# Kernel optimization log

Measured on AMD Instinct MI355X. Metric: run time of the kernel, lower is better.

Reference implementation:

```python
import jax, jax.numpy as jnp
import numpy as np

HIDDEN = 2048
N_EXPERTS = 8
TOP_K = 2
MOE_INTER = 1408
NORM_TOPK = False  # config.norm_topk_prob


def setup_inputs() -> dict:
    key = jax.random.key(0)
    k0, k1, k2, k3, k4 = jax.random.split(key, 5)
    hidden_states = jax.random.normal(k0, (2, 2048, HIDDEN), dtype=jnp.float32)
    # router gate: nn.Linear(hidden, num_experts, bias=False) -> store as [H, E]
    gate_w = jax.random.normal(k1, (HIDDEN, N_EXPERTS), dtype=jnp.float32) * 0.02
    # per-expert MLP weights, stacked over experts (Linear is x @ W.T, stored pre-transposed)
    w_gate = jax.random.normal(k2, (N_EXPERTS, HIDDEN, MOE_INTER), dtype=jnp.float32) * 0.02
    w_up = jax.random.normal(k3, (N_EXPERTS, HIDDEN, MOE_INTER), dtype=jnp.float32) * 0.02
    w_down = jax.random.normal(k4, (N_EXPERTS, MOE_INTER, HIDDEN), dtype=jnp.float32) * 0.02
    return {"hidden_states": hidden_states, "gate_w": gate_w,
            "w_gate": w_gate, "w_up": w_up, "w_down": w_down}


def reference(hidden_states, gate_w, w_gate, w_up, w_down):
    B, S, H = hidden_states.shape
    x = hidden_states.reshape(-1, H)                      # [T, H]
    T = x.shape[0]
    router_logits = x @ gate_w                            # [T, E]
    probs = jax.nn.softmax(router_logits.astype(jnp.float32), axis=-1)
    routing_weights, selected = jax.lax.top_k(probs, TOP_K)  # [T, K], [T, K]
    if NORM_TOPK:
        routing_weights = routing_weights / routing_weights.sum(-1, keepdims=True)
    routing_weights = routing_weights.astype(x.dtype)
    # dense combine weights [T, E]: scatter top-k weights to expert slots
    combine = jnp.zeros((T, N_EXPERTS), dtype=x.dtype)
    combine = combine.at[jnp.arange(T)[:, None], selected].add(routing_weights)
    # run all experts densely (reference form of gather-MLP-scatter)
    g = jnp.einsum('th,ehf->tef', x, w_gate)              # [T, E, F]
    u = jnp.einsum('th,ehf->tef', x, w_up)
    h = jax.nn.silu(g) * u
    y = jnp.einsum('tef,efh->teh', h, w_down)             # [T, E, H]
    out = jnp.einsum('te,teh->th', combine, y)            # [T, H]
    return out
```

## Files before the change

### kernel.cpp

```cpp
#include <hip/hip_runtime.h>
#include <hip/hip_bf16.h>

#define HID  2048
#define NEXP 8
#define FINT 1408
#define TM   256
#define BK   32
#define GU_NPAN 88
#define DN_NPAN 64

typedef __bf16 bf16_t;
typedef __bf16 bf16x8 __attribute__((ext_vector_type(8)));
typedef float  f32x4  __attribute__((ext_vector_type(4)));

#define AS1 __attribute__((address_space(1)))
#define AS3 __attribute__((address_space(3)))

__device__ __forceinline__ void gll16(const void* g, void* l) {
    __builtin_amdgcn_global_load_lds((const AS1 void*)g, (AS3 void*)l, 16, 0, 0);
}

#define VMCNT4() asm volatile("s_waitcnt vmcnt(4)" ::: "memory")
#define VMCNT0() asm volatile("s_waitcnt vmcnt(0)" ::: "memory")
#define LGKM0()  asm volatile("s_waitcnt lgkmcnt(0)" ::: "memory")
#define SB0() __builtin_amdgcn_sched_barrier(0)

__global__ __launch_bounds__(64) void router_kernel(
    const float* __restrict__ x, const float* __restrict__ gw,
    int* __restrict__ cnt, int* __restrict__ topk_id, float* __restrict__ topk_w,
    bf16_t* __restrict__ xb, int T)
{
    int t = blockIdx.x;
    if (t >= T) return;
    int lane = threadIdx.x;
    float acc[NEXP];
#pragma unroll
    for (int e = 0; e < NEXP; ++e) acc[e] = 0.f;
    const float* xr = x + (size_t)t * HID;
    bf16_t* xo = xb + (size_t)t * HID;
    for (int i = lane; i < HID; i += 64) {
        float xv = xr[i];
        xo[i] = (bf16_t)xv;
        const float4* g4 = (const float4*)(gw + (size_t)i * NEXP);
        float4 a = g4[0], b = g4[1];
        acc[0] += xv * a.x; acc[1] += xv * a.y; acc[2] += xv * a.z; acc[3] += xv * a.w;
        acc[4] += xv * b.x; acc[5] += xv * b.y; acc[6] += xv * b.z; acc[7] += xv * b.w;
    }
#pragma unroll
    for (int d = 1; d < 64; d <<= 1) {
#pragma unroll
        for (int e = 0; e < NEXP; ++e) acc[e] += __shfl_xor(acc[e], d, 64);
    }
    float mx = acc[0];
#pragma unroll
    for (int e = 1; e < NEXP; ++e) mx = fmaxf(mx, acc[e]);
    float p[NEXP]; float s = 0.f;
#pragma unroll
    for (int e = 0; e < NEXP; ++e) { p[e] = expf(acc[e] - mx); s += p[e]; }
    float inv = 1.f / s;
    int i1 = 0;
#pragma unroll
    for (int e = 1; e < NEXP; ++e) if (acc[e] > acc[i1]) i1 = e;
    int i2 = (i1 == 0) ? 1 : 0;
#pragma unroll
    for (int e = 0; e < NEXP; ++e) if (e != i1 && acc[e] > acc[i2]) i2 = e;
    if (lane == 0) {
        topk_id[t * 2 + 0] = i1; topk_id[t * 2 + 1] = i2;
        topk_w[t * 2 + 0] = p[i1] * inv; topk_w[t * 2 + 1] = p[i2] * inv;
        atomicAdd(&cnt[i1], 1); atomicAdd(&cnt[i2], 1);
    }
}

__global__ void offsets_kernel(const int* __restrict__ cnt, int* __restrict__ offs,
                               int* __restrict__ gbase, int* __restrict__ gcount,
                               int* __restrict__ dbase, int* __restrict__ dcount,
                               int* __restrict__ gu, int* __restrict__ dn)
{
    __shared__ int gc[8], dc[8];
    int tid = threadIdx.x;
    if (tid == 0) {
        int s = 0;
        for (int e = 0; e < NEXP; ++e) { offs[e] = s; s += cnt[e]; }
        offs[NEXP] = s;
    }
    if (tid < 8) {
        int c = 0;
        for (int p = tid; p < GU_NPAN; p += 8) { int e = p / 11; c += (cnt[e] + TM - 1) / TM; }
        gc[tid] = c;
    } else if (tid < 16) {
        int x = tid - 8, c = 0;
        for (int p = x; p < DN_NPAN; p += 8) { int e = p >> 3; c += (cnt[e] + TM - 1) / TM; }
        dc[x] = c;
    }
    __syncthreads();
    if (tid < 8) {
        int base = 0;
        for (int i = 0; i < tid; ++i) base += gc[i];
        gbase[tid] = base; gcount[tid] = gc[tid];
        int k = base;
        for (int p = tid; p < GU_NPAN; p += 8) {
            int e = p / 11, fp = p - e * 11;
            int nt = (cnt[e] + TM - 1) / TM;
            for (int t = 0; t < nt; ++t) gu[k++] = (e << 10) | (fp << 6) | t;
        }
    } else if (tid < 16) {
        int x = tid - 8;
        int base = 0;
        for (int i = 0; i < x; ++i) base += dc[i];
        dbase[x] = base; dcount[x] = dc[x];
        int k = base;
        for (int p = x; p < DN_NPAN; p += 8) {
            int e = p >> 3, hp = p & 7;
            int nt = (cnt[e] + TM - 1) / TM;
            for (int t = 0; t < nt; ++t) dn[k++] = (e << 10) | (hp << 6) | t;
        }
    }
}

__global__ void scatter_kernel(
    const int* __restrict__ topk_id, const int* __restrict__ offs, int* __restrict__ fill,
    int* __restrict__ tok, int* __restrict__ slot_of, int T)
{
    int t = blockIdx.x * blockDim.x + threadIdx.x;
    if (t >= T) return;
#pragma unroll
    for (int k = 0; k < 2; ++k) {
        int e = topk_id[t * 2 + k];
        int pos = atomicAdd(&fill[e], 1);
        int slot = offs[e] + pos;
        tok[slot] = t;
        slot_of[t * 2 + k] = slot;
    }
}

__global__ __launch_bounds__(256) void cvt3_kernel(
    const float* __restrict__ wg, const float* __restrict__ wu, const float* __restrict__ wd,
    bf16_t* __restrict__ wgb, bf16_t* __restrict__ wub, bf16_t* __restrict__ wdb)
{
    const int per = NEXP * (HID / 64) * (FINT / 64);
    int b = blockIdx.x;
    const float* in; bf16_t* outb; int R, C;
    if (b < per)            { in = wg; outb = wgb; R = HID;  C = FINT; }
    else if (b < 2 * per)   { b -= per; in = wu; outb = wub; R = HID;  C = FINT; }
    else                    { b -= 2 * per; in = wd; outb = wdb; R = FINT; C = HID; }

    int tilesC = C >> 6;
    int perE = (R >> 6) * tilesC;
    int e = b / perE;
    int rem = b - e * perE;
    int tr = rem / tilesC, tc = rem - tr * tilesC;
    const float* src = in + (size_t)e * R * C + (size_t)(tr * 64) * C + tc * 64;
    bf16_t* dst = outb + (size_t)e * R * C + (size_t)(tc * 64) * R + tr * 64;

    __shared__ float tile[64][65];
    int tid = threadIdx.x;
    int rr = tid >> 4;
    int cc = (tid & 15) * 4;
#pragma unroll
    for (int i = 0; i < 4; ++i) {
        float4 v = *(const float4*)(src + (size_t)(rr + i * 16) * C + cc);
        tile[rr + i * 16][cc + 0] = v.x; tile[rr + i * 16][cc + 1] = v.y;
        tile[rr + i * 16][cc + 2] = v.z; tile[rr + i * 16][cc + 3] = v.w;
    }
    __syncthreads();
    int oc = tid >> 2;
    int og = (tid & 3) * 16;
    bf16_t* dp = dst + (size_t)oc * R + og;
    bf16x8 o0, o1;
#pragma unroll
    for (int j = 0; j < 8; ++j) { o0[j] = (bf16_t)tile[og + j][oc]; o1[j] = (bf16_t)tile[og + 8 + j][oc]; }
    *(bf16x8*)dp = o0;
    *(bf16x8*)(dp + 8) = o1;
}

__global__ __launch_bounds__(512, 2) void gateup3_kernel(
    const bf16_t* __restrict__ xb, const bf16_t* __restrict__ wgb, const bf16_t* __restrict__ wub,
    const int* __restrict__ offs, const int* __restrict__ tok,
    const int* __restrict__ gbase, const int* __restrict__ gcount, const int* __restrict__ gu,
    bf16_t* __restrict__ h_buf)
{
    __shared__ bf16_t smem[49152];
    const int tid = threadIdx.x;
    const int lane = tid & 63, w = tid >> 6;
    const int wm = w >> 1, wn = w & 1;
    const int lr = lane & 15, lg = lane >> 4;
    const int rl = lane >> 2;
    const int sw8 = ((lane & 3) ^ ((lane >> 3) & 3)) * 8;
    const int ksw = (lg ^ ((lr >> 1) & 3)) * 8;

    const int xcd = blockIdx.x & 7, slot = blockIdx.x >> 3;
    const int icnt = gcount[xcd], ib = gbase[xcd];

    for (int ii = slot; ii < icnt; ii += 32) {
        const int it = gu[ib + ii];
        const int e = it >> 10, fp = (it >> 6) & 15, tr = it & 63;
        const int seg0 = offs[e];
        const int rbase = tr * TM;
        const int nvalid = min(offs[e + 1] - seg0 - rbase, TM);
        const int row0 = seg0 + rbase;
        const int f0 = fp * 128;

        const bf16_t* aP[2];
#pragma unroll
        for (int i = 0; i < 2; ++i) {
            int r = (w * 2 + i) * 16 + rl;
            int tk = tok[row0 + min(r, nvalid - 1)];
            aP[i] = xb + (size_t)tk * HID + sw8;
        }
        const bf16_t* bP[2];
#pragma unroll
        for (int i = 0; i < 2; ++i) {
            int br = (w * 2 + i) * 16 + rl;
            const bf16_t* W = (br < 128) ? wgb : wub;
            bP[i] = W + ((size_t)e * FINT + f0 + (br & 127)) * HID + sw8;
        }

        f32x4 acc[4][8];
#pragma unroll
        for (int mi = 0; mi < 4; ++mi)
#pragma unroll
            for (int ni = 0; ni < 8; ++ni) acc[mi][ni] = (f32x4){0.f, 0.f, 0.f, 0.f};

        auto STAGE_A = [&](int b, int kt) {
            int k0 = kt * BK;
            bf16_t* A = smem + b * 8192;
            gll16(aP[0] + k0, A + (w * 2 + 0) * 512);
            gll16(aP[1] + k0, A + (w * 2 + 1) * 512);
        };
        auto STAGE_B = [&](int b, int kt) {
            int k0 = kt * BK;
            bf16_t* B = smem + 24576 + b * 8192;
            gll16(bP[0] + k0, B + (w * 2 + 0) * 512);
            gll16(bP[1] + k0, B + (w * 2 + 1) * 512);
        };

        const int NK = HID / BK;
        STAGE_A(0, 0); STAGE_B(0, 0); STAGE_A(1, 1); STAGE_B(1, 1);
        int c0 = 0, c1 = 1, c2 = 2;
        for (int kt = 0; kt < NK; ++kt) {
            SB0();
            if (kt + 1 < NK) { VMCNT4(); } else { VMCNT0(); }
            __builtin_amdgcn_s_barrier();
            SB0();
            const bf16_t* A = smem + c0 * 8192;
            const bf16_t* B = smem + 24576 + c0 * 8192;
            if (kt + 2 < NK) STAGE_A(c2, kt + 2);
            bf16x8 afr[4], bfr[4];
#pragma unroll
            for (int mi = 0; mi < 4; ++mi)
                afr[mi] = *(const bf16x8*)&A[(wm * 64 + mi * 16 + lr) * BK + ksw];
#pragma unroll
            for (int ni = 0; ni < 4; ++ni)
                bfr[ni] = *(const bf16x8*)&B[(wn * 128 + ni * 16 + lr) * BK + ksw];
            LGKM0(); SB0();
            __builtin_amdgcn_s_setprio(1);
#pragma unroll
            for (int mi = 0; mi < 4; ++mi)
#pragma unroll
                for (int ni = 0; ni < 4; ++ni)
                    acc[mi][ni] = __builtin_amdgcn_mfma_f32_16x16x32_bf16(afr[mi], bfr[ni], acc[mi][ni], 0, 0, 0);
            __builtin_amdgcn_s_setprio(0);
            SB0();
            if (kt + 2 < NK) STAGE_B(c2, kt + 2);
#pragma unroll
            for (int ni = 0; ni < 4; ++ni)
                bfr[ni] = *(const bf16x8*)&B[(wn * 128 + (ni + 4) * 16 + lr) * BK + ksw];
            LGKM0(); SB0();
            __builtin_amdgcn_s_setprio(1);
#pragma unroll
            for (int mi = 0; mi < 4; ++mi)
#pragma unroll
                for (int ni = 0; ni < 4; ++ni)
                    acc[mi][ni + 4] = __builtin_amdgcn_mfma_f32_16x16x32_bf16(afr[mi], bfr[ni], acc[mi][ni + 4], 0, 0, 0);
            __builtin_amdgcn_s_setprio(0);
            SB0();
            int t = c0; c0 = c1; c1 = c2; c2 = t;
        }
        __syncthreads();

        if (wn == 1) {
#pragma unroll
            for (int mi = 0; mi < 4; ++mi)
#pragma unroll
                for (int ni = 0; ni < 8; ++ni)
#pragma unroll
                    for (int rr = 0; rr < 4; ++rr) {
                        int row = wm * 64 + mi * 16 + lg * 4 + rr;
                        int col = ni * 16 + lr;
                        smem[row * 128 + col] = (bf16_t)acc[mi][ni][rr];
                    }
        }
        __syncthreads();
        if (wn == 0) {
#pragma unroll
            for (int mi = 0; mi < 4; ++mi)
#pragma unroll
                for (int ni = 0; ni < 8; ++ni)
#pragma unroll
                    for (int rr = 0; rr < 4; ++rr) {
                        int row = wm * 64 + mi * 16 + lg * 4 + rr;
                        int col = ni * 16 + lr;
                        float g = acc[mi][ni][rr];
                        float u = (float)smem[row * 128 + col];
                        float h = (g / (1.f + __expf(-g))) * u;
                        if (row < nvalid)
                            h_buf[(size_t)(row0 + row) * FINT + f0 + col] = (bf16_t)h;
                    }
        }
        __syncthreads();
    }
}

__global__ __launch_bounds__(512, 2) void down3_kernel(
    const bf16_t* __restrict__ h_buf, const bf16_t* __restrict__ wdb,
    const int* __restrict__ offs,
    const int* __restrict__ dbase, const int* __restrict__ dcount, const int* __restrict__ dn,
    bf16_t* __restrict__ y_buf)
{
    __shared__ bf16_t smem[49152];
    const int tid = threadIdx.x;
    const int lane = tid & 63, w = tid >> 6;
    const int wm = w >> 1, wn = w & 1;
    const int lr = lane & 15, lg = lane >> 4;
    const int rl = lane >> 2;
    const int sw8 = ((lane & 3) ^ ((lane >> 3) & 3)) * 8;
    const int ksw = (lg ^ ((lr >> 1) & 3)) * 8;

    const int xcd = blockIdx.x & 7, slot = blockIdx.x >> 3;
    const int icnt = dcount[xcd], ib = dbase[xcd];

    for (int ii = slot; ii < icnt; ii += 32) {
        const int it = dn[ib + ii];
        const int e = it >> 10, hp = (it >> 6) & 15, tr = it & 63;
        const int seg0 = offs[e];
        const int rbase = tr * TM;
        const int nvalid = min(offs[e + 1] - seg0 - rbase, TM);
        const int row0 = seg0 + rbase;
        const int h0 = hp * 256;

        const bf16_t* aP[2];
#pragma unroll
        for (int i = 0; i < 2; ++i) {
            int r = (w * 2 + i) * 16 + rl;
            aP[i] = h_buf + (size_t)(row0 + r) * FINT + sw8;
        }
        const bf16_t* bP[2];
#pragma unroll
        for (int i = 0; i < 2; ++i) {
            int br = (w * 2 + i) * 16 + rl;
            bP[i] = wdb + ((size_t)e * HID + h0 + br) * FINT + sw8;
        }

        f32x4 acc[4][8];
#pragma unroll
        for (int mi = 0; mi < 4; ++mi)
#pragma unroll
            for (int ni = 0; ni < 8; ++ni) acc[mi][ni] = (f32x4){0.f, 0.f, 0.f, 0.f};

        auto STAGE_A = [&](int b, int kt) {
            int k0 = kt * BK;
            bf16_t* A = smem + b * 8192;
            gll16(aP[0] + k0, A + (w * 2 + 0) * 512);
            gll16(aP[1] + k0, A + (w * 2 + 1) * 512);
        };
        auto STAGE_B = [&](int b, int kt) {
            int k0 = kt * BK;
            bf16_t* B = smem + 24576 + b * 8192;
            gll16(bP[0] + k0, B + (w * 2 + 0) * 512);
            gll16(bP[1] + k0, B + (w * 2 + 1) * 512);
        };

        const int NK = FINT / BK;
        STAGE_A(0, 0); STAGE_B(0, 0); STAGE_A(1, 1); STAGE_B(1, 1);
        int c0 = 0, c1 = 1, c2 = 2;
        for (int kt = 0; kt < NK; ++kt) {
            SB0();
            if (kt + 1 < NK) { VMCNT4(); } else { VMCNT0(); }
            __builtin_amdgcn_s_barrier();
            SB0();
            const bf16_t* A = smem + c0 * 8192;
            const bf16_t* B = smem + 24576 + c0 * 8192;
            if (kt + 2 < NK) STAGE_A(c2, kt + 2);
            bf16x8 afr[4], bfr[4];
#pragma unroll
            for (int mi = 0; mi < 4; ++mi)
                afr[mi] = *(const bf16x8*)&A[(wm * 64 + mi * 16 + lr) * BK + ksw];
#pragma unroll
            for (int ni = 0; ni < 4; ++ni)
                bfr[ni] = *(const bf16x8*)&B[(wn * 128 + ni * 16 + lr) * BK + ksw];
            LGKM0(); SB0();
            __builtin_amdgcn_s_setprio(1);
#pragma unroll
            for (int mi = 0; mi < 4; ++mi)
#pragma unroll
                for (int ni = 0; ni < 4; ++ni)
                    acc[mi][ni] = __builtin_amdgcn_mfma_f32_16x16x32_bf16(afr[mi], bfr[ni], acc[mi][ni], 0, 0, 0);
            __builtin_amdgcn_s_setprio(0);
            SB0();
            if (kt + 2 < NK) STAGE_B(c2, kt + 2);
#pragma unroll
            for (int ni = 0; ni < 4; ++ni)
                bfr[ni] = *(const bf16x8*)&B[(wn * 128 + (ni + 4) * 16 + lr) * BK + ksw];
            LGKM0(); SB0();
            __builtin_amdgcn_s_setprio(1);
#pragma unroll
            for (int mi = 0; mi < 4; ++mi)
#pragma unroll
                for (int ni = 0; ni < 4; ++ni)
                    acc[mi][ni + 4] = __builtin_amdgcn_mfma_f32_16x16x32_bf16(afr[mi], bfr[ni], acc[mi][ni + 4], 0, 0, 0);
            __builtin_amdgcn_s_setprio(0);
            SB0();
            int t = c0; c0 = c1; c1 = c2; c2 = t;
        }

#pragma unroll
        for (int mi = 0; mi < 4; ++mi)
#pragma unroll
            for (int ni = 0; ni < 8; ++ni)
#pragma unroll
                for (int rr = 0; rr < 4; ++rr) {
                    int row = wm * 64 + mi * 16 + lg * 4 + rr;
                    int col = wn * 128 + ni * 16 + lr;
                    if (row < nvalid)
                        y_buf[(size_t)(row0 + row) * HID + h0 + col] = (bf16_t)acc[mi][ni][rr];
                }
        __syncthreads();
    }
}

__global__ __launch_bounds__(256) void combine_kernel(
    const bf16_t* __restrict__ y, const int* __restrict__ slot_of,
    const float* __restrict__ topk_w, float* __restrict__ out, int T)
{
    int t = blockIdx.x;
    int tid = threadIdx.x;
    int s0 = slot_of[t * 2], s1 = slot_of[t * 2 + 1];
    float w0 = topk_w[t * 2], w1 = topk_w[t * 2 + 1];
    const bf16x8* y0 = (const bf16x8*)(y + (size_t)s0 * HID);
    const bf16x8* y1 = (const bf16x8*)(y + (size_t)s1 * HID);
    bf16x8 v0 = y0[tid], v1 = y1[tid];
    float* op = out + (size_t)t * HID + tid * 8;
#pragma unroll
    for (int j = 0; j < 8; ++j)
        op[j] = w0 * (float)v0[j] + w1 * (float)v1[j];
}

extern "C" void kernel_launch(void* const* d_in, const int* in_sizes, int n_in,
                              void* d_out, int out_size, void* d_ws, size_t ws_size,
                              hipStream_t stream)
{
    const float* x  = (const float*)d_in[0];
    const float* gw = (const float*)d_in[1];
    const float* wg = (const float*)d_in[2];
    const float* wu = (const float*)d_in[3];
    const float* wd = (const float*)d_in[4];
    float* out = (float*)d_out;
    int T = in_sizes[0] / HID;
    int S2 = 2 * T;

    char* base = (char*)d_ws;
    int* cnt     = (int*)base;
    int* fill    = cnt + 8;
    int* offs    = cnt + 16;
    int* gbase   = cnt + 32;
    int* gcount  = cnt + 40;
    int* dbase   = cnt + 48;
    int* dcount  = cnt + 56;
    int* gu      = cnt + 64;
    int* dnl     = cnt + 576;
    int* topk_id = cnt + 960;
    float* topk_w = (float*)(topk_id + S2);
    int* tok     = (int*)(topk_w + S2);
    int* slot_of = tok + S2 + 256;
    size_t small_end = (size_t)((char*)(slot_of + S2) - base);
    size_t cur = (small_end + 255) & ~(size_t)255;
    auto take = [&](size_t bytes) -> size_t {
        size_t o = cur; cur += bytes; cur = (cur + 255) & ~(size_t)255; return o;
    };
    size_t wbytes = (size_t)NEXP * HID * FINT * 2;
    size_t o_xb  = take((size_t)T * HID * 2);
    size_t o_wgb = take(wbytes);
    size_t o_wub = take(wbytes);
    size_t o_wdb = take(wbytes);
    size_t o_h   = take((size_t)(S2 + 256) * FINT * 2);
    size_t o_y   = take((size_t)(S2 + 256) * HID * 2);
    (void)ws_size;

    bf16_t* xb    = (bf16_t*)(base + o_xb);
    bf16_t* wgb   = (bf16_t*)(base + o_wgb);
    bf16_t* wub   = (bf16_t*)(base + o_wub);
    bf16_t* wdb   = (bf16_t*)(base + o_wdb);
    bf16_t* h_buf = (bf16_t*)(base + o_h);
    bf16_t* y_buf = (bf16_t*)(base + o_y);

    hipMemsetAsync(base, 0, 64, stream);

    router_kernel<<<T, 64, 0, stream>>>(x, gw, cnt, topk_id, topk_w, xb, T);
    offsets_kernel<<<1, 64, 0, stream>>>(cnt, offs, gbase, gcount, dbase, dcount, gu, dnl);
    scatter_kernel<<<(T + 255) / 256, 256, 0, stream>>>(topk_id, offs, fill, tok, slot_of, T);

    int gridW = 3 * NEXP * (HID / 64) * (FINT / 64);
    cvt3_kernel<<<gridW, 256, 0, stream>>>(wg, wu, wd, wgb, wub, wdb);

    gateup3_kernel<<<256, 512, 0, stream>>>(xb, wgb, wub, offs, tok, gbase, gcount, gu, h_buf);
    down3_kernel<<<256, 512, 0, stream>>>(h_buf, wdb, offs, dbase, dcount, dnl, y_buf);
    combine_kernel<<<T, 256, 0, stream>>>(y_buf, slot_of, topk_w, out, T);
}
```

Before: 469.4 us.

## Restructure grouped GEMMs to BK=64 quadrant-pipelined double buffering with 2x4 warp grid

Both the gate/up and down grouped GEMM kernels move from a BK=32 triple-buffered loop to BK=64 double buffering with 128 KB of LDS. Each k-step is split into four quadrant sub-tiles whose loads are staged in between the MFMA phases. Warps are rearranged as a 2x4 grid with a 128x64 tile per warp, and the LDS swizzle becomes 8-way XOR. The aim is fewer barriers per unit of MFMA work and less wasted global-load issue, at the cost of dropping to one block per CU. The router kernel also switches to float4 loads of x.

```diff
diff --git a/kernel.cpp b/kernel.cpp
--- a/kernel.cpp
+++ b/kernel.cpp
@@ -5,7 +5,6 @@
 #define NEXP 8
 #define FINT 1408
 #define TM   256
-#define BK   32
 #define GU_NPAN 88
 #define DN_NPAN 64
 
@@ -20,8 +19,9 @@
     __builtin_amdgcn_global_load_lds((const AS1 void*)g, (AS3 void*)l, 16, 0, 0);
 }
 
-#define VMCNT4() asm volatile("s_waitcnt vmcnt(4)" ::: "memory")
-#define VMCNT0() asm volatile("s_waitcnt vmcnt(0)" ::: "memory")
+#define VM4() asm volatile("s_waitcnt vmcnt(4)" ::: "memory")
+#define VM2() asm volatile("s_waitcnt vmcnt(2)" ::: "memory")
+#define VM0() asm volatile("s_waitcnt vmcnt(0)" ::: "memory")
 #define LGKM0()  asm volatile("s_waitcnt lgkmcnt(0)" ::: "memory")
 #define SB0() __builtin_amdgcn_sched_barrier(0)
 
@@ -38,13 +38,18 @@
     for (int e = 0; e < NEXP; ++e) acc[e] = 0.f;
     const float* xr = x + (size_t)t * HID;
     bf16_t* xo = xb + (size_t)t * HID;
-    for (int i = lane; i < HID; i += 64) {
-        float xv = xr[i];
-        xo[i] = (bf16_t)xv;
-        const float4* g4 = (const float4*)(gw + (size_t)i * NEXP);
-        float4 a = g4[0], b = g4[1];
-        acc[0] += xv * a.x; acc[1] += xv * a.y; acc[2] += xv * a.z; acc[3] += xv * a.w;
-        acc[4] += xv * b.x; acc[5] += xv * b.y; acc[6] += xv * b.z; acc[7] += xv * b.w;
+    for (int i0 = lane * 4; i0 < HID; i0 += 256) {
+        float4 xv = *(const float4*)(xr + i0);
+        bf16_t b4[4] = {(bf16_t)xv.x, (bf16_t)xv.y, (bf16_t)xv.z, (bf16_t)xv.w};
+        *(uint2*)(xo + i0) = *(uint2*)b4;
+        float xs[4] = {xv.x, xv.y, xv.z, xv.w};
+#pragma unroll
+        for (int u = 0; u < 4; ++u) {
+            const float4* g4 = (const float4*)(gw + (size_t)(i0 + u) * NEXP);
+            float4 a = g4[0], b = g4[1];
+            acc[0] += xs[u] * a.x; acc[1] += xs[u] * a.y; acc[2] += xs[u] * a.z; acc[3] += xs[u] * a.w;
+            acc[4] += xs[u] * b.x; acc[5] += xs[u] * b.y; acc[6] += xs[u] * b.z; acc[7] += xs[u] * b.w;
+        }
     }
 #pragma unroll
     for (int d = 1; d < 64; d <<= 1) {
@@ -173,20 +178,24 @@
     *(bf16x8*)(dp + 8) = o1;
 }
 
-__global__ __launch_bounds__(512, 2) void gateup3_kernel(
+
+__global__ __launch_bounds__(512, 1) void gateup4_kernel(
     const bf16_t* __restrict__ xb, const bf16_t* __restrict__ wgb, const bf16_t* __restrict__ wub,
     const int* __restrict__ offs, const int* __restrict__ tok,
     const int* __restrict__ gbase, const int* __restrict__ gcount, const int* __restrict__ gu,
     bf16_t* __restrict__ h_buf)
 {
-    __shared__ bf16_t smem[49152];
+    __shared__ bf16_t smem[65536];
     const int tid = threadIdx.x;
     const int lane = tid & 63, w = tid >> 6;
-    const int wm = w >> 1, wn = w & 1;
+    const int wr = w >> 2, wc = w & 3;
     const int lr = lane & 15, lg = lane >> 4;
-    const int rl = lane >> 2;
-    const int sw8 = ((lane & 3) ^ ((lane >> 3) & 3)) * 8;
-    const int ksw = (lg ^ ((lr >> 1) & 3)) * 8;
+    const int sw7 = lr & 7;
+    const int ksrc = ((lane & 7) ^ ((lane >> 3) & 7)) * 8;
+    int iS[2];
+#pragma unroll
+    for (int j = 0; j < 2; ++j) iS[j] = w * 16 + j * 8 + (lane >> 3);
+    const int dA[2] = { (w * 128 + 0) * 8, (w * 128 + 64) * 8 };
 
     const int xcd = blockIdx.x & 7, slot = blockIdx.x >> 3;
     const int icnt = gcount[xcd], ib = gbase[xcd];
@@ -200,107 +209,109 @@
         const int row0 = seg0 + rbase;
         const int f0 = fp * 128;
 
-        const bf16_t* aP[2];
-#pragma unroll
-        for (int i = 0; i < 2; ++i) {
-            int r = (w * 2 + i) * 16 + rl;
-            int tk = tok[row0 + min(r, nvalid - 1)];
-            aP[i] = xb + (size_t)tk * HID + sw8;
-        }
-        const bf16_t* bP[2];
-#pragma unroll
-        for (int i = 0; i < 2; ++i) {
-            int br = (w * 2 + i) * 16 + rl;
-            const bf16_t* W = (br < 128) ? wgb : wub;
-            bP[i] = W + ((size_t)e * FINT + f0 + (br & 127)) * HID + sw8;
-        }
-
-        f32x4 acc[4][8];
-#pragma unroll
-        for (int mi = 0; mi < 4; ++mi)
-#pragma unroll
-            for (int ni = 0; ni < 8; ++ni) acc[mi][ni] = (f32x4){0.f, 0.f, 0.f, 0.f};
-
-        auto STAGE_A = [&](int b, int kt) {
-            int k0 = kt * BK;
-            bf16_t* A = smem + b * 8192;
-            gll16(aP[0] + k0, A + (w * 2 + 0) * 512);
-            gll16(aP[1] + k0, A + (w * 2 + 1) * 512);
+        const bf16_t* aSrc[2][2];
+        const bf16_t* bSrc[2];
+#pragma unroll
+        for (int j = 0; j < 2; ++j) {
+            int rA0 = ((iS[j] >> 6) << 7) + (iS[j] & 63);
+#pragma unroll
+            for (int mh = 0; mh < 2; ++mh) {
+                int rA = rA0 + mh * 64;
+                int tk = tok[row0 + min(rA, nvalid - 1)];
+                aSrc[j][mh] = xb + (size_t)tk * HID + ksrc;
+            }
+            int rB = ((iS[j] >> 5) << 6) + (iS[j] & 31);
+            const bf16_t* W = (rB < 128) ? wgb : wub;
+            bSrc[j] = W + ((size_t)e * FINT + f0 + (rB & 127)) * HID + ksrc;
+        }
+
+        f32x4 acc[8][4];
+#pragma unroll
+        for (int mf = 0; mf < 8; ++mf)
+#pragma unroll
+            for (int nf = 0; nf < 4; ++nf) acc[mf][nf] = (f32x4){0.f, 0.f, 0.f, 0.f};
+
+        auto SG_A = [&](int bb, int kt, int mh) {
+#pragma unroll
+            for (int j = 0; j < 2; ++j)
+                gll16(aSrc[j][mh] + kt * 64, &smem[bb * 16384 + mh * 8192 + dA[j]]);
         };
-        auto STAGE_B = [&](int b, int kt) {
-            int k0 = kt * BK;
-            bf16_t* B = smem + 24576 + b * 8192;
-            gll16(bP[0] + k0, B + (w * 2 + 0) * 512);
-            gll16(bP[1] + k0, B + (w * 2 + 1) * 512);
+        auto SG_B = [&](int bb, int kt, int nh) {
+#pragma unroll
+            for (int j = 0; j < 2; ++j)
+                gll16(bSrc[j] + (size_t)nh * 32 * HID + kt * 64, &smem[32768 + bb * 16384 + nh * 8192 + dA[j]]);
         };
 
-        const int NK = HID / BK;
-        STAGE_A(0, 0); STAGE_B(0, 0); STAGE_A(1, 1); STAGE_B(1, 1);
-        int c0 = 0, c1 = 1, c2 = 2;
+#define GU_READ_MFMA(BB, MH, NH)                                                              \
+        {                                                                                     \
+            bf16x8 afr[4][2], bfr[2][2];                                                      \
+            _Pragma("unroll")                                                                 \
+            for (int m = 0; m < 4; ++m)                                                       \
+                _Pragma("unroll")                                                             \
+                for (int ks = 0; ks < 2; ++ks)                                                \
+                    afr[m][ks] = *(const bf16x8*)&smem[(BB) * 16384 + (MH) * 8192 +           \
+                        (wr * 64 + m * 16 + lr) * 64 + (((ks * 4 + lg) ^ sw7)) * 8];          \
+            _Pragma("unroll")                                                                 \
+            for (int n = 0; n < 2; ++n)                                                       \
+                _Pragma("unroll")                                                             \
+                for (int ks = 0; ks < 2; ++ks)                                                \
+                    bfr[n][ks] = *(const bf16x8*)&smem[32768 + (BB) * 16384 + (NH) * 8192 +   \
+                        (wc * 32 + n * 16 + lr) * 64 + (((ks * 4 + lg) ^ sw7)) * 8];          \
+            LGKM0(); SB0();                                                                   \
+            __builtin_amdgcn_s_setprio(1);                                                    \
+            _Pragma("unroll")                                                                 \
+            for (int m = 0; m < 4; ++m)                                                       \
+                _Pragma("unroll")                                                             \
+                for (int n = 0; n < 2; ++n)                                                   \
+                    _Pragma("unroll")                                                         \
+                    for (int ks = 0; ks < 2; ++ks)                                            \
+                        acc[(MH) * 4 + m][(NH) * 2 + n] = __builtin_amdgcn_mfma_f32_16x16x32_bf16( \
+                            afr[m][ks], bfr[n][ks], acc[(MH) * 4 + m][(NH) * 2 + n], 0, 0, 0); \
+            __builtin_amdgcn_s_setprio(0);                                                    \
+        }
+
+        const int NK = HID / 64;
+        SG_B(0, 0, 0); SG_A(0, 0, 0); SG_A(0, 0, 1); SG_B(0, 0, 1);
         for (int kt = 0; kt < NK; ++kt) {
-            SB0();
-            if (kt + 1 < NK) { VMCNT4(); } else { VMCNT0(); }
-            __builtin_amdgcn_s_barrier();
-            SB0();
-            const bf16_t* A = smem + c0 * 8192;
-            const bf16_t* B = smem + 24576 + c0 * 8192;
-            if (kt + 2 < NK) STAGE_A(c2, kt + 2);
-            bf16x8 afr[4], bfr[4];
-#pragma unroll
-            for (int mi = 0; mi < 4; ++mi)
-                afr[mi] = *(const bf16x8*)&A[(wm * 64 + mi * 16 + lr) * BK + ksw];
-#pragma unroll
-            for (int ni = 0; ni < 4; ++ni)
-                bfr[ni] = *(const bf16x8*)&B[(wn * 128 + ni * 16 + lr) * BK + ksw];
-            LGKM0(); SB0();
-            __builtin_amdgcn_s_setprio(1);
-#pragma unroll
-            for (int mi = 0; mi < 4; ++mi)
-#pragma unroll
-                for (int ni = 0; ni < 4; ++ni)
-                    acc[mi][ni] = __builtin_amdgcn_mfma_f32_16x16x32_bf16(afr[mi], bfr[ni], acc[mi][ni], 0, 0, 0);
-            __builtin_amdgcn_s_setprio(0);
-            SB0();
-            if (kt + 2 < NK) STAGE_B(c2, kt + 2);
-#pragma unroll
-            for (int ni = 0; ni < 4; ++ni)
-                bfr[ni] = *(const bf16x8*)&B[(wn * 128 + (ni + 4) * 16 + lr) * BK + ksw];
-            LGKM0(); SB0();
-            __builtin_amdgcn_s_setprio(1);
-#pragma unroll
-            for (int mi = 0; mi < 4; ++mi)
-#pragma unroll
-                for (int ni = 0; ni < 4; ++ni)
-                    acc[mi][ni + 4] = __builtin_amdgcn_mfma_f32_16x16x32_bf16(afr[mi], bfr[ni], acc[mi][ni + 4], 0, 0, 0);
-            __builtin_amdgcn_s_setprio(0);
-            SB0();
-            int t = c0; c0 = c1; c1 = c2; c2 = t;
+            const int bb = kt & 1, nb = bb ^ 1;
+            const bool nl = (kt + 1 < NK);
+            SB0(); LGKM0(); VM4(); __builtin_amdgcn_s_barrier(); SB0();
+            if (nl) SG_B(nb, kt + 1, 0);
+            GU_READ_MFMA(bb, 0, 0);
+            SB0(); LGKM0(); if (nl) { VM4(); } else { VM2(); } __builtin_amdgcn_s_barrier(); SB0();
+            if (nl) SG_A(nb, kt + 1, 0);
+            GU_READ_MFMA(bb, 1, 0);
+            SB0(); LGKM0(); if (nl) { VM4(); } else { VM0(); } __builtin_amdgcn_s_barrier(); SB0();
+            if (nl) SG_A(nb, kt + 1, 1);
+            GU_READ_MFMA(bb, 0, 1);
+            if (nl) SG_B(nb, kt + 1, 1);
+            GU_READ_MFMA(bb, 1, 1);
         }
         __syncthreads();
 
-        if (wn == 1) {
-#pragma unroll
-            for (int mi = 0; mi < 4; ++mi)
-#pragma unroll
-                for (int ni = 0; ni < 8; ++ni)
+        if (wc >= 2) {
+#pragma unroll
+            for (int mf = 0; mf < 8; ++mf)
+#pragma unroll
+                for (int nf = 0; nf < 4; ++nf)
 #pragma unroll
                     for (int rr = 0; rr < 4; ++rr) {
-                        int row = wm * 64 + mi * 16 + lg * 4 + rr;
-                        int col = ni * 16 + lr;
-                        smem[row * 128 + col] = (bf16_t)acc[mi][ni][rr];
+                        int row = wr * 128 + mf * 16 + lg * 4 + rr;
+                        int col = (wc - 2) * 64 + nf * 16 + lr;
+                        smem[row * 128 + col] = (bf16_t)acc[mf][nf][rr];
                     }
         }
         __syncthreads();
-        if (wn == 0) {
-#pragma unroll
-            for (int mi = 0; mi < 4; ++mi)
-#pragma unroll
-                for (int ni = 0; ni < 8; ++ni)
+        if (wc < 2) {
+#pragma unroll
+            for (int mf = 0; mf < 8; ++mf)
+#pragma unroll
+                for (int nf = 0; nf < 4; ++nf)
 #pragma unroll
                     for (int rr = 0; rr < 4; ++rr) {
-                        int row = wm * 64 + mi * 16 + lg * 4 + rr;
-                        int col = ni * 16 + lr;
-                        float g = acc[mi][ni][rr];
+                        int row = wr * 128 + mf * 16 + lg * 4 + rr;
+                        int col = wc * 64 + nf * 16 + lr;
+                        float g = acc[mf][nf][rr];
                         float u = (float)smem[row * 128 + col];
                         float h = (g / (1.f + __expf(-g))) * u;
                         if (row < nvalid)
@@ -309,22 +320,26 @@
         }
         __syncthreads();
     }
-}
-
-__global__ __launch_bounds__(512, 2) void down3_kernel(
+#undef GU_READ_MFMA
+}
+
+__global__ __launch_bounds__(512, 1) void down4_kernel(
     const bf16_t* __restrict__ h_buf, const bf16_t* __restrict__ wdb,
     const int* __restrict__ offs,
     const int* __restrict__ dbase, const int* __restrict__ dcount, const int* __restrict__ dn,
     bf16_t* __restrict__ y_buf)
 {
-    __shared__ bf16_t smem[49152];
+    __shared__ bf16_t smem[65536];
     const int tid = threadIdx.x;
     const int lane = tid & 63, w = tid >> 6;
-    const int wm = w >> 1, wn = w & 1;
+    const int wr = w >> 2, wc = w & 3;
     const int lr = lane & 15, lg = lane >> 4;
-    const int rl = lane >> 2;
-    const int sw8 = ((lane & 3) ^ ((lane >> 3) & 3)) * 8;
-    const int ksw = (lg ^ ((lr >> 1) & 3)) * 8;
+    const int sw7 = lr & 7;
+    const int ksrc = ((lane & 7) ^ ((lane >> 3) & 7)) * 8;
+    int iS[2];
+#pragma unroll
+    for (int j = 0; j < 2; ++j) iS[j] = w * 16 + j * 8 + (lane >> 3);
+    const int dA[2] = { (w * 128 + 0) * 8, (w * 128 + 64) * 8 };
 
     const int xcd = blockIdx.x & 7, slot = blockIdx.x >> 3;
     const int icnt = dcount[xcd], ib = dbase[xcd];
@@ -338,94 +353,95 @@
         const int row0 = seg0 + rbase;
         const int h0 = hp * 256;
 
-        const bf16_t* aP[2];
-#pragma unroll
-        for (int i = 0; i < 2; ++i) {
-            int r = (w * 2 + i) * 16 + rl;
-            aP[i] = h_buf + (size_t)(row0 + r) * FINT + sw8;
-        }
-        const bf16_t* bP[2];
-#pragma unroll
-        for (int i = 0; i < 2; ++i) {
-            int br = (w * 2 + i) * 16 + rl;
-            bP[i] = wdb + ((size_t)e * HID + h0 + br) * FINT + sw8;
-        }
-
-        f32x4 acc[4][8];
-#pragma unroll
-        for (int mi = 0; mi < 4; ++mi)
-#pragma unroll
-            for (int ni = 0; ni < 8; ++ni) acc[mi][ni] = (f32x4){0.f, 0.f, 0.f, 0.f};
-
-        auto STAGE_A = [&](int b, int kt) {
-            int k0 = kt * BK;
-            bf16_t* A = smem + b * 8192;
-            gll16(aP[0] + k0, A + (w * 2 + 0) * 512);
-            gll16(aP[1] + k0, A + (w * 2 + 1) * 512);
+        const bf16_t* aSrc[2][2];
+        const bf16_t* bSrc[2];
+#pragma unroll
+        for (int j = 0; j < 2; ++j) {
+            int rA0 = ((iS[j] >> 6) << 7) + (iS[j] & 63);
+#pragma unroll
+            for (int mh = 0; mh < 2; ++mh)
+                aSrc[j][mh] = h_buf + (size_t)(row0 + rA0 + mh * 64) * FINT + ksrc;
+            int rB = ((iS[j] >> 5) << 6) + (iS[j] & 31);
+            bSrc[j] = wdb + ((size_t)e * HID + h0 + rB) * FINT + ksrc;
+        }
+
+        f32x4 acc[8][4];
+#pragma unroll
+        for (int mf = 0; mf < 8; ++mf)
+#pragma unroll
+            for (int nf = 0; nf < 4; ++nf) acc[mf][nf] = (f32x4){0.f, 0.f, 0.f, 0.f};
+
+        auto SG_A = [&](int bb, int kt, int mh) {
+#pragma unroll
+            for (int j = 0; j < 2; ++j)
+                gll16(aSrc[j][mh] + kt * 64, &smem[bb * 16384 + mh * 8192 + dA[j]]);
         };
-        auto STAGE_B = [&](int b, int kt) {
-            int k0 = kt * BK;
-            bf16_t* B = smem + 24576 + b * 8192;
-            gll16(bP[0] + k0, B + (w * 2 + 0) * 512);
-            gll16(bP[1] + k0, B + (w * 2 + 1) * 512);
+        auto SG_B = [&](int bb, int kt, int nh) {
+#pragma unroll
+            for (int j = 0; j < 2; ++j)
+                gll16(bSrc[j] + (size_t)nh * 32 * FINT + kt * 64, &smem[32768 + bb * 16384 + nh * 8192 + dA[j]]);
         };
 
-        const int NK = FINT / BK;
-        STAGE_A(0, 0); STAGE_B(0, 0); STAGE_A(1, 1); STAGE_B(1, 1);
-        int c0 = 0, c1 = 1, c2 = 2;
+#define DN_READ_MFMA(BB, MH, NH)                                                              \
+        {                                                                                     \
+            bf16x8 afr[4][2], bfr[2][2];                                                      \
+            _Pragma("unroll")                                                                 \
+            for (int m = 0; m < 4; ++m)                                                       \
+                _Pragma("unroll")                                                             \
+                for (int ks = 0; ks < 2; ++ks)                                                \
+                    afr[m][ks] = *(const bf16x8*)&smem[(BB) * 16384 + (MH) * 8192 +           \
+                        (wr * 64 + m * 16 + lr) * 64 + (((ks * 4 + lg) ^ sw7)) * 8];          \
+            _Pragma("unroll")                                                                 \
+            for (int n = 0; n < 2; ++n)                                                       \
+                _Pragma("unroll")                                                             \
+                for (int ks = 0; ks < 2; ++ks)                                                \
+                    bfr[n][ks] = *(const bf16x8*)&smem[32768 + (BB) * 16384 + (NH) * 8192 +   \
+                        (wc * 32 + n * 16 + lr) * 64 + (((ks * 4 + lg) ^ sw7)) * 8];          \
+            LGKM0(); SB0();                                                                   \
+            __builtin_amdgcn_s_setprio(1);                                                    \
+            _Pragma("unroll")                                                                 \
+            for (int m = 0; m < 4; ++m)                                                       \
+                _Pragma("unroll")                                                             \
+                for (int n = 0; n < 2; ++n)                                                   \
+                    _Pragma("unroll")                                                         \
+                    for (int ks = 0; ks < 2; ++ks)                                            \
+                        acc[(MH) * 4 + m][(NH) * 2 + n] = __builtin_amdgcn_mfma_f32_16x16x32_bf16( \
+                            afr[m][ks], bfr[n][ks], acc[(MH) * 4 + m][(NH) * 2 + n], 0, 0, 0); \
+            __builtin_amdgcn_s_setprio(0);                                                    \
+        }
+
+        const int NK = FINT / 64;
+        SG_B(0, 0, 0); SG_A(0, 0, 0); SG_A(0, 0, 1); SG_B(0, 0, 1);
         for (int kt = 0; kt < NK; ++kt) {
-            SB0();
-            if (kt + 1 < NK) { VMCNT4(); } else { VMCNT0(); }
-            __builtin_amdgcn_s_barrier();
-            SB0();
-            const bf16_t* A = smem + c0 * 8192;
-            const bf16_t* B = smem + 24576 + c0 * 8192;
-            if (kt + 2 < NK) STAGE_A(c2, kt + 2);
-            bf16x8 afr[4], bfr[4];
-#pragma unroll
-            for (int mi = 0; mi < 4; ++mi)
-                afr[mi] = *(const bf16x8*)&A[(wm * 64 + mi * 16 + lr) * BK + ksw];
-#pragma unroll
-            for (int ni = 0; ni < 4; ++ni)
-                bfr[ni] = *(const bf16x8*)&B[(wn * 128 + ni * 16 + lr) * BK + ksw];
-            LGKM0(); SB0();
-            __builtin_amdgcn_s_setprio(1);
-#pragma unroll
-            for (int mi = 0; mi < 4; ++mi)
-#pragma unroll
-                for (int ni = 0; ni < 4; ++ni)
-                    acc[mi][ni] = __builtin_amdgcn_mfma_f32_16x16x32_bf16(afr[mi], bfr[ni], acc[mi][ni], 0, 0, 0);
-            __builtin_amdgcn_s_setprio(0);
-            SB0();
-            if (kt + 2 < NK) STAGE_B(c2, kt + 2);
-#pragma unroll
-            for (int ni = 0; ni < 4; ++ni)
-                bfr[ni] = *(const bf16x8*)&B[(wn * 128 + (ni + 4) * 16 + lr) * BK + ksw];
-            LGKM0(); SB0();
-            __builtin_amdgcn_s_setprio(1);
-#pragma unroll
-            for (int mi = 0; mi < 4; ++mi)
-#pragma unroll
-                for (int ni = 0; ni < 4; ++ni)
-                    acc[mi][ni + 4] = __builtin_amdgcn_mfma_f32_16x16x32_bf16(afr[mi], bfr[ni], acc[mi][ni + 4], 0, 0, 0);
-            __builtin_amdgcn_s_setprio(0);
-            SB0();
-            int t = c0; c0 = c1; c1 = c2; c2 = t;
-        }
-
-#pragma unroll
-        for (int mi = 0; mi < 4; ++mi)
-#pragma unroll
-            for (int ni = 0; ni < 8; ++ni)
+            const int bb = kt & 1, nb = bb ^ 1;
+            const bool nl = (kt + 1 < NK);
+            SB0(); LGKM0(); VM4(); __builtin_amdgcn_s_barrier(); SB0();
+            if (nl) SG_B(nb, kt + 1, 0);
+            DN_READ_MFMA(bb, 0, 0);
+            SB0(); LGKM0(); if (nl) { VM4(); } else { VM2(); } __builtin_amdgcn_s_barrier(); SB0();
+            if (nl) SG_A(nb, kt + 1, 0);
+            DN_READ_MFMA(bb, 1, 0);
+            SB0(); LGKM0(); if (nl) { VM4(); } else { VM0(); } __builtin_amdgcn_s_barrier(); SB0();
+            if (nl) SG_A(nb, kt + 1, 1);
+            DN_READ_MFMA(bb, 0, 1);
+            if (nl) SG_B(nb, kt + 1, 1);
+            DN_READ_MFMA(bb, 1, 1);
+        }
+
+#pragma unroll
+        for (int mf = 0; mf < 8; ++mf)
+#pragma unroll
+            for (int nf = 0; nf < 4; ++nf)
 #pragma unroll
                 for (int rr = 0; rr < 4; ++rr) {
-                    int row = wm * 64 + mi * 16 + lg * 4 + rr;
-                    int col = wn * 128 + ni * 16 + lr;
+                    int row = wr * 128 + mf * 16 + lg * 4 + rr;
+                    int col = wc * 64 + nf * 16 + lr;
                     if (row < nvalid)
-                        y_buf[(size_t)(row0 + row) * HID + h0 + col] = (bf16_t)acc[mi][ni][rr];
+                        y_buf[(size_t)(row0 + row) * HID + h0 + col] = (bf16_t)acc[mf][nf][rr];
                 }
         __syncthreads();
     }
+#undef DN_READ_MFMA
 }
 
 __global__ __launch_bounds__(256) void combine_kernel(
@@ -502,7 +518,7 @@
     int gridW = 3 * NEXP * (HID / 64) * (FINT / 64);
     cvt3_kernel<<<gridW, 256, 0, stream>>>(wg, wu, wd, wgb, wub, wdb);
 
-    gateup3_kernel<<<256, 512, 0, stream>>>(xb, wgb, wub, offs, tok, gbase, gcount, gu, h_buf);
-    down3_kernel<<<256, 512, 0, stream>>>(h_buf, wdb, offs, dbase, dcount, dnl, y_buf);
+    gateup4_kernel<<<256, 512, 0, stream>>>(xb, wgb, wub, offs, tok, gbase, gcount, gu, h_buf);
+    down4_kernel<<<256, 512, 0, stream>>>(h_buf, wdb, offs, dbase, dcount, dnl, y_buf);
     combine_kernel<<<T, 256, 0, stream>>>(y_buf, slot_of, topk_w, out, T);
 }
```

After: 479.6 us. 1.02x slower.
